# Optimization experiments

Measured on AMD Instinct MI355X. Metric: run time of the kernel, lower is better.

The kernel has to match this reference:

```python
import jax, jax.numpy as jnp
import numpy as np

N_NODES = 100000
N_EDGES = 1600000
IN_F = 64
OUT_F = 32
NEG_SLOPE = 0.2


def setup_inputs() -> dict:
    key = jax.random.key(0)
    k = jax.random.split(key, 6)
    x = jax.random.normal(k[0], (N_NODES, IN_F), dtype=jnp.float32)
    edge_index = jax.random.randint(k[1], (2, N_EDGES), 0, N_NODES, dtype=jnp.int64)
    W = jax.random.normal(k[2], (IN_F, OUT_F), dtype=jnp.float32) * 0.1
    att_src = jax.random.normal(k[3], (OUT_F,), dtype=jnp.float32) * 0.1
    att_dst = jax.random.normal(k[4], (OUT_F,), dtype=jnp.float32) * 0.1
    bias = jax.random.normal(k[5], (OUT_F,), dtype=jnp.float32) * 0.1
    return {"x": x, "edge_index": edge_index, "W": W,
            "att_src": att_src, "att_dst": att_dst, "bias": bias}


def reference(x, edge_index, W, att_src, att_dst, bias):
    N = x.shape[0]
    # Linear projection (single head, concat=True -> [N, OUT_F])
    h = x @ W  # [N, C]
    a_src = h @ att_src  # [N] per-node source attention logit contribution
    a_dst = h @ att_dst  # [N] per-node destination contribution
    # add self loops (PyG GATConv default add_self_loops=True)
    loop = jnp.arange(N, dtype=edge_index.dtype)
    src = jnp.concatenate([edge_index[0], loop])  # [E+N] message senders
    dst = jnp.concatenate([edge_index[1], loop])  # [E+N] message receivers
    # attention logits per edge, LeakyReLU(alpha_src[j] + alpha_dst[i])
    e = jax.nn.leaky_relu(a_src[src] + a_dst[dst], NEG_SLOPE)
    # segment softmax over incoming edges of each destination node
    m = jax.ops.segment_max(e, dst, num_segments=N)  # every node has a self loop
    ex = jnp.exp(e - m[dst])
    denom = jax.ops.segment_sum(ex, dst, num_segments=N)
    alpha = ex / denom[dst]  # [E+N]
    # weighted scatter-add of source features into destinations
    out = jax.ops.segment_sum(h[src] * alpha[:, None], dst, num_segments=N)
    out = out + bias
    # GATLayer activation='relu'
    return jax.nn.relu(out)
```

## Files before the change

kernel.cpp:

```cpp
#include <hip/hip_runtime.h>
#include <hip/hip_fp16.h>
#include <math.h>

#define IN_F 64
#define OUT_F 32
#define NEG_SLOPE 0.2f

#define BK_SHIFT 7
#define BK 128
#define NBMAX 1024
#define NBLKA 256
#define PSTAGE 10

typedef _Float16 half8_t __attribute__((ext_vector_type(8)));
typedef float float4_t __attribute__((ext_vector_type(4)));

__device__ __forceinline__ float leaky(float v) {
    return (v > 0.0f) ? v : NEG_SLOPE * v;
}

__device__ __forceinline__ int incScan256(int v, int tid, int* wsum) {
    const int lane = tid & 63, wid = tid >> 6;
    #pragma unroll
    for (int m = 1; m < 64; m <<= 1) {
        int u = __shfl_up(v, m);
        if (lane >= m) v += u;
    }
    if (lane == 63) wsum[wid] = v;
    __syncthreads();
    int add = 0;
    for (int k = 0; k < wid; ++k) add += wsum[k];
    __syncthreads();
    return v + add;
}

__device__ __forceinline__ int incScan512(int v, int tid, int* wsum) {
    const int lane = tid & 63, wid = tid >> 6;
    #pragma unroll
    for (int m = 1; m < 64; m <<= 1) {
        int u = __shfl_up(v, m);
        if (lane >= m) v += u;
    }
    if (lane == 63) wsum[wid] = v;
    __syncthreads();
    int add = 0;
    for (int k = 0; k < wid; ++k) add += wsum[k];
    __syncthreads();
    return v + add;
}

__global__ __launch_bounds__(256) void k_projhist(
        const float* __restrict__ x, const float* __restrict__ W,
        const float* __restrict__ att_src, const float* __restrict__ att_dst,
        __half2* __restrict__ h2, float* __restrict__ asrc, float* __restrict__ adst,
        const int* __restrict__ dst, int* __restrict__ hist,
        int N, int NB, int E, int epb, int PB) {
    __shared__ int smem[2560];
    const int tid = threadIdx.x;

    if (blockIdx.x >= PB) {
        int* lh = smem;
        const int blk = blockIdx.x - PB;
        for (int i = tid; i < NB; i += 256) lh[i] = 0;
        __syncthreads();
        const int e0 = blk * epb, e1 = min(E, e0 + epb);
        for (int e = e0 + tid; e < e1; e += 256) atomicAdd(&lh[dst[e] >> BK_SHIFT], 1);
        __syncthreads();
        for (int b = tid; b < NB; b += 256) hist[(size_t)b * NBLKA + blk] = lh[b];
        return;
    }

    const int wv   = tid >> 6;
    const int lane = tid & 63;
    const int m    = lane & 15;
    const int quad = lane >> 4;
    const int node0 = (blockIdx.x * 4 + wv) * 16;
    if (node0 >= N) return;

    const int kb = quad * 8;
    half8_t b00, b01, b10, b11;
    #pragma unroll
    for (int j = 0; j < 8; ++j) {
        b00[j] = (_Float16)W[(kb + j) * OUT_F + m];
        b01[j] = (_Float16)W[(32 + kb + j) * OUT_F + m];
        b10[j] = (_Float16)W[(kb + j) * OUT_F + 16 + m];
        b11[j] = (_Float16)W[(32 + kb + j) * OUT_F + 16 + m];
    }
    const int row = min(node0 + m, N - 1);
    const float* xr = x + (size_t)row * IN_F + kb;
    float4_t xa = *(const float4_t*)(xr);
    float4_t xb = *(const float4_t*)(xr + 4);
    float4_t xc = *(const float4_t*)(xr + 32);
    float4_t xd = *(const float4_t*)(xr + 36);
    half8_t a0, a1;
    #pragma unroll
    for (int j = 0; j < 4; ++j) {
        a0[j] = (_Float16)xa[j]; a0[4 + j] = (_Float16)xb[j];
        a1[j] = (_Float16)xc[j]; a1[4 + j] = (_Float16)xd[j];
    }
    float4_t acc0 = {0.f, 0.f, 0.f, 0.f};
    float4_t acc1 = {0.f, 0.f, 0.f, 0.f};
    acc0 = __builtin_amdgcn_mfma_f32_16x16x32_f16(a0, b00, acc0, 0, 0, 0);
    acc0 = __builtin_amdgcn_mfma_f32_16x16x32_f16(a1, b01, acc0, 0, 0, 0);
    acc1 = __builtin_amdgcn_mfma_f32_16x16x32_f16(a0, b10, acc1, 0, 0, 0);
    acc1 = __builtin_amdgcn_mfma_f32_16x16x32_f16(a1, b11, acc1, 0, 0, 0);

    const float aS0 = att_src[m], aS1 = att_src[16 + m];
    const float aD0 = att_dst[m], aD1 = att_dst[16 + m];
    #pragma unroll
    for (int r = 0; r < 4; ++r) {
        const int node = node0 + quad * 4 + r;
        float h0 = acc0[r], h1 = acc1[r];
        float h0p = __shfl_xor(h0, 1);
        float h1p = __shfl_xor(h1, 1);
        if (node < N && (m & 1) == 0) {
            __half2 hv;
            hv.x = __float2half_rn(h0); hv.y = __float2half_rn(h0p);
            h2[(size_t)node * 16 + (m >> 1)] = hv;
            __half2 hw;
            hw.x = __float2half_rn(h1); hw.y = __float2half_rn(h1p);
            h2[(size_t)node * 16 + 8 + (m >> 1)] = hw;
        }
        float vs = h0 * aS0 + h1 * aS1;
        float vd = h0 * aD0 + h1 * aD1;
        #pragma unroll
        for (int mm = 1; mm < 16; mm <<= 1) {
            vs += __shfl_xor(vs, mm);
            vd += __shfl_xor(vd, mm);
        }
        if (node < N && m == 0) {
            asrc[node] = vs;
            adst[node] = vd;
        }
    }
}

__global__ __launch_bounds__(256) void k_scan1(int* __restrict__ hist,
                                               int* __restrict__ bsum, int NB) {
    __shared__ int wsum[4];
    const int b = blockIdx.x, tid = threadIdx.x;
    int v = hist[(size_t)b * NBLKA + tid];
    const int inc = incScan256(v, tid, wsum);
    hist[(size_t)b * NBLKA + tid] = inc - v;
    if (tid == 255) bsum[b] = inc;
}

__global__ __launch_bounds__(512) void k_bpart(const int* __restrict__ src,
                                               const int* __restrict__ dst,
                                               const int* __restrict__ hist,
                                               const int* __restrict__ bsum,
                                               int* __restrict__ recs,
                                               int NB, int E, int epb) {
    __shared__ int tt[NBMAX];
    __shared__ int lcur[NBMAX];
    __shared__ int wsum[8];
    const int tid = threadIdx.x, blk = blockIdx.x;
    for (int i = tid; i < NBMAX; i += 512) tt[i] = (i < NB) ? bsum[i] : 0;
    __syncthreads();
    {
        int a0 = tt[tid * 2], a1 = tt[tid * 2 + 1];
        int s = a0 + a1;
        int inc = incScan512(s, tid, wsum);
        int run = inc - s;
        tt[tid * 2] = run; run += a0;
        tt[tid * 2 + 1] = run;
    }
    __syncthreads();
    for (int b = tid; b < NB; b += 512)
        lcur[b] = hist[(size_t)b * NBLKA + blk] + tt[b];
    __syncthreads();
    const int e0 = blk * epb, e1 = min(E, e0 + epb);
    for (int e = e0 + tid; e < e1; e += 512) {
        int s = src[e];
        int d = dst[e];
        int p = atomicAdd(&lcur[d >> BK_SHIFT], 1);
        recs[p] = ((d & (BK - 1)) << 17) | s;
    }
}

__global__ __launch_bounds__(256) void k_place(const int* __restrict__ recs,
                                               const int* __restrict__ bsum,
                                               int* __restrict__ cnt,
                                               int* __restrict__ offs,
                                               int* __restrict__ col,
                                               int NB, int E, int N) {
    __shared__ int tt[NBMAX];
    __shared__ int fineCnt[BK];
    __shared__ int cur[BK];
    __shared__ int wsum[4];
    const int b = blockIdx.x, tid = threadIdx.x;
    for (int i = tid; i < NBMAX; i += 256) tt[i] = (i < NB) ? bsum[i] : 0;
    __syncthreads();
    {
        int a0 = tt[tid * 4], a1 = tt[tid * 4 + 1], a2 = tt[tid * 4 + 2], a3 = tt[tid * 4 + 3];
        int s = a0 + a1 + a2 + a3;
        int inc = incScan256(s, tid, wsum);
        int run = inc - s;
        tt[tid * 4] = run;     run += a0;
        tt[tid * 4 + 1] = run; run += a1;
        tt[tid * 4 + 2] = run; run += a2;
        tt[tid * 4 + 3] = run;
    }
    __syncthreads();
    const int cb0 = tt[b];
    const int cb1 = (b + 1 < NB) ? tt[b + 1] : E;
    const int count = cb1 - cb0;
    int myrec[PSTAGE];
    if (tid < BK) fineCnt[tid] = 0;
    __syncthreads();
    #pragma unroll
    for (int k = 0; k < PSTAGE; ++k) {
        int i = tid + k * 256;
        if (i < count) {
            int v = recs[cb0 + i];
            myrec[k] = v;
            atomicAdd(&fineCnt[v >> 17], 1);
        }
    }
    for (int i = tid + PSTAGE * 256; i < count; i += 256)
        atomicAdd(&fineCnt[recs[cb0 + i] >> 17], 1);
    __syncthreads();
    const int v0 = (tid < BK) ? fineCnt[tid] : 0;
    const int inc = incScan256(v0, tid, wsum);
    const int excl = inc - v0;
    if (tid < BK) {
        const int node = (b << BK_SHIFT) + tid;
        if (node < N) {
            cnt[node]  = v0;
            offs[node] = cb0 + excl;
        }
        cur[tid] = cb0 + excl;
    }
    __syncthreads();
    #pragma unroll
    for (int k = 0; k < PSTAGE; ++k) {
        int i = tid + k * 256;
        if (i < count) {
            int r = myrec[k];
            int p = atomicAdd(&cur[r >> 17], 1);
            col[p] = r & 0x1FFFF;
        }
    }
    for (int i = tid + PSTAGE * 256; i < count; i += 256) {
        int r = recs[cb0 + i];
        int p = atomicAdd(&cur[r >> 17], 1);
        col[p] = r & 0x1FFFF;
    }
}

__global__ void k_gather(const int* __restrict__ col, const int* __restrict__ offs,
                         const int* __restrict__ cnt, const float* __restrict__ asrc,
                         const float* __restrict__ adst, const __half2* __restrict__ h2,
                         const float* __restrict__ bias, float* __restrict__ out, int N) {
    int t = blockIdx.x * 256 + threadIdx.x;
    int n = t >> 6;
    if (n >= N) return;
    const int lane = t & 63;
    const int g  = lane >> 4;
    const int c2 = lane & 15;
    const float adst_n = adst[n];
    float l = 0.0f, accx = 0.0f, accy = 0.0f;
    if (g == 0) {
        float p = __expf(leaky(asrc[n] + adst_n));
        float2 hv = __half22float2(h2[(size_t)n * 16 + c2]);
        l = p; accx = p * hv.x; accy = p * hv.y;
    }
    const int off = offs[n];
    const int deg = cnt[n];
    const int q = (deg + 3) >> 2;
    int j = off + g * q;
    const int jend = min(j + q, off + deg);
    for (; j < jend; j += 4) {
        const int last = jend - 1;
        int i1 = min(j + 1, last), i2 = min(j + 2, last), i3 = min(j + 3, last);
        int s0 = col[j], s1 = col[i1], s2 = col[i2], s3 = col[i3];
        float a0 = asrc[s0], a1 = asrc[s1], a2 = asrc[s2], a3 = asrc[s3];
        float2 h0 = __half22float2(h2[(size_t)s0 * 16 + c2]);
        float2 h1 = __half22float2(h2[(size_t)s1 * 16 + c2]);
        float2 hv2 = __half22float2(h2[(size_t)s2 * 16 + c2]);
        float2 h3 = __half22float2(h2[(size_t)s3 * 16 + c2]);
        float p0 = __expf(leaky(a0 + adst_n));
        float p1 = (j + 1 < jend) ? __expf(leaky(a1 + adst_n)) : 0.0f;
        float p2 = (j + 2 < jend) ? __expf(leaky(a2 + adst_n)) : 0.0f;
        float p3 = (j + 3 < jend) ? __expf(leaky(a3 + adst_n)) : 0.0f;
        l += (p0 + p1) + (p2 + p3);
        accx += p0 * h0.x + p1 * h1.x + p2 * hv2.x + p3 * h3.x;
        accy += p0 * h0.y + p1 * h1.y + p2 * hv2.y + p3 * h3.y;
    }
    l    += __shfl_xor(l, 16);    l    += __shfl_xor(l, 32);
    accx += __shfl_xor(accx, 16); accx += __shfl_xor(accx, 32);
    accy += __shfl_xor(accy, 16); accy += __shfl_xor(accy, 32);
    if (g == 0) {
        float inv = 1.0f / l;
        float2 bb = ((const float2*)bias)[c2];
        float2 o;
        o.x = fmaxf(accx * inv + bb.x, 0.0f);
        o.y = fmaxf(accy * inv + bb.y, 0.0f);
        ((float2*)out)[(size_t)n * 16 + c2] = o;
    }
}

extern "C" void kernel_launch(void* const* d_in, const int* in_sizes, int n_in,
                              void* d_out, int out_size, void* d_ws, size_t ws_size,
                              hipStream_t stream) {
    const float* x        = (const float*)d_in[0];
    const int*   eidx     = (const int*)d_in[1];
    const float* W        = (const float*)d_in[2];
    const float* att_src  = (const float*)d_in[3];
    const float* att_dst  = (const float*)d_in[4];
    const float* bias     = (const float*)d_in[5];
    float* out = (float*)d_out;

    const int N = in_sizes[0] / IN_F;
    const int E = in_sizes[1] / 2;
    const int* src = eidx;
    const int* dst = eidx + E;

    const int NB  = (N + BK - 1) >> BK_SHIFT;
    const int epb = (E + NBLKA - 1) / NBLKA;

    int* u = (int*)d_ws;
    size_t o = 0;
    __half2* h2   = (__half2*)(u + o); o += (size_t)N * 16;
    float*   asrc = (float*)(u + o);   o += N;
    float*   adst = (float*)(u + o);   o += N;
    int*     cnt  = u + o;             o += N;
    int*     offs = u + o;             o += N;
    int*     hist = u + o;             o += (size_t)NB * NBLKA;
    int*     bsum = u + o;             o += NBMAX;
    int*     col  = u + o;             o += E;
    int*     recs = u + o;             o += E;

    const int PB = (N + 63) / 64;
    const int gatherBlocks = ((size_t)N * 64 + 255) / 256;

    k_projhist<<<PB + NBLKA, 256, 0, stream>>>(x, W, att_src, att_dst, h2, asrc, adst,
                                               dst, hist, N, NB, E, epb, PB);
    k_scan1<<<NB, 256, 0, stream>>>(hist, bsum, NB);
    k_bpart<<<NBLKA, 512, 0, stream>>>(src, dst, hist, bsum, recs, NB, E, epb);
    k_place<<<NB, 256, 0, stream>>>(recs, bsum, cnt, offs, col, NB, E, N);
    k_gather<<<gatherBlocks, 256, 0, stream>>>(col, offs, cnt, asrc, adst, h2, bias, out, N);
}
```

Baseline: 169.0 us.

## Replace fine CSR placement and gather with bucket-level shared-memory atomic aggregation

```diff
diff --git a/kernel.cpp b/kernel.cpp
--- a/kernel.cpp
+++ b/kernel.cpp
@@ -10,13 +10,18 @@
 #define BK 128
 #define NBMAX 1024
 #define NBLKA 256
-#define PSTAGE 10
 
 typedef _Float16 half8_t __attribute__((ext_vector_type(8)));
 typedef float float4_t __attribute__((ext_vector_type(4)));
+typedef int int4_t __attribute__((ext_vector_type(4)));
 
 __device__ __forceinline__ float leaky(float v) {
     return (v > 0.0f) ? v : NEG_SLOPE * v;
+}
+
+__device__ __forceinline__ float2 h2f(int w) {
+    __half2 h = *reinterpret_cast<__half2*>(&w);
+    return __half22float2(h);
 }
 
 __device__ __forceinline__ int incScan256(int v, int tid, int* wsum) {
@@ -150,6 +155,7 @@
                                                const int* __restrict__ hist,
                                                const int* __restrict__ bsum,
                                                int* __restrict__ recs,
+                                               int* __restrict__ boff,
                                                int NB, int E, int epb) {
     __shared__ int tt[NBMAX];
     __shared__ int lcur[NBMAX];
@@ -166,6 +172,10 @@
         tt[tid * 2 + 1] = run;
     }
     __syncthreads();
+    if (blk == 0) {
+        for (int b = tid; b < NB; b += 512) boff[b] = tt[b];
+        if (tid == 0) boff[NB] = E;
+    }
     for (int b = tid; b < NB; b += 512)
         lcur[b] = hist[(size_t)b * NBLKA + blk] + tt[b];
     __syncthreads();
@@ -178,125 +188,75 @@
     }
 }
 
-__global__ __launch_bounds__(256) void k_place(const int* __restrict__ recs,
-                                               const int* __restrict__ bsum,
-                                               int* __restrict__ cnt,
-                                               int* __restrict__ offs,
-                                               int* __restrict__ col,
-                                               int NB, int E, int N) {
-    __shared__ int tt[NBMAX];
-    __shared__ int fineCnt[BK];
-    __shared__ int cur[BK];
-    __shared__ int wsum[4];
+__global__ __launch_bounds__(512) void k_agg(const int* __restrict__ recs,
+                                             const int* __restrict__ boff,
+                                             const float* __restrict__ asrc,
+                                             const float* __restrict__ adst,
+                                             const __half2* __restrict__ h2,
+                                             const float* __restrict__ bias,
+                                             float* __restrict__ out,
+                                             int NB, int E, int N) {
+    __shared__ float acc[BK * 33];
+    __shared__ float adl[BK];
     const int b = blockIdx.x, tid = threadIdx.x;
-    for (int i = tid; i < NBMAX; i += 256) tt[i] = (i < NB) ? bsum[i] : 0;
-    __syncthreads();
-    {
-        int a0 = tt[tid * 4], a1 = tt[tid * 4 + 1], a2 = tt[tid * 4 + 2], a3 = tt[tid * 4 + 3];
-        int s = a0 + a1 + a2 + a3;
-        int inc = incScan256(s, tid, wsum);
-        int run = inc - s;
-        tt[tid * 4] = run;     run += a0;
-        tt[tid * 4 + 1] = run; run += a1;
-        tt[tid * 4 + 2] = run; run += a2;
-        tt[tid * 4 + 3] = run;
-    }
-    __syncthreads();
-    const int cb0 = tt[b];
-    const int cb1 = (b + 1 < NB) ? tt[b + 1] : E;
-    const int count = cb1 - cb0;
-    int myrec[PSTAGE];
-    if (tid < BK) fineCnt[tid] = 0;
-    __syncthreads();
-    #pragma unroll
-    for (int k = 0; k < PSTAGE; ++k) {
-        int i = tid + k * 256;
-        if (i < count) {
-            int v = recs[cb0 + i];
-            myrec[k] = v;
-            atomicAdd(&fineCnt[v >> 17], 1);
-        }
-    }
-    for (int i = tid + PSTAGE * 256; i < count; i += 256)
-        atomicAdd(&fineCnt[recs[cb0 + i] >> 17], 1);
-    __syncthreads();
-    const int v0 = (tid < BK) ? fineCnt[tid] : 0;
-    const int inc = incScan256(v0, tid, wsum);
-    const int excl = inc - v0;
+    const int node0 = b << BK_SHIFT;
+
+    for (int i = tid; i < BK * 33; i += 512) acc[i] = 0.0f;
     if (tid < BK) {
-        const int node = (b << BK_SHIFT) + tid;
-        if (node < N) {
-            cnt[node]  = v0;
-            offs[node] = cb0 + excl;
-        }
-        cur[tid] = cb0 + excl;
-    }
-    __syncthreads();
-    #pragma unroll
-    for (int k = 0; k < PSTAGE; ++k) {
-        int i = tid + k * 256;
-        if (i < count) {
-            int r = myrec[k];
-            int p = atomicAdd(&cur[r >> 17], 1);
-            col[p] = r & 0x1FFFF;
-        }
-    }
-    for (int i = tid + PSTAGE * 256; i < count; i += 256) {
-        int r = recs[cb0 + i];
-        int p = atomicAdd(&cur[r >> 17], 1);
-        col[p] = r & 0x1FFFF;
-    }
-}
-
-__global__ void k_gather(const int* __restrict__ col, const int* __restrict__ offs,
-                         const int* __restrict__ cnt, const float* __restrict__ asrc,
-                         const float* __restrict__ adst, const __half2* __restrict__ h2,
-                         const float* __restrict__ bias, float* __restrict__ out, int N) {
-    int t = blockIdx.x * 256 + threadIdx.x;
-    int n = t >> 6;
-    if (n >= N) return;
-    const int lane = t & 63;
-    const int g  = lane >> 4;
-    const int c2 = lane & 15;
-    const float adst_n = adst[n];
-    float l = 0.0f, accx = 0.0f, accy = 0.0f;
-    if (g == 0) {
-        float p = __expf(leaky(asrc[n] + adst_n));
-        float2 hv = __half22float2(h2[(size_t)n * 16 + c2]);
-        l = p; accx = p * hv.x; accy = p * hv.y;
-    }
-    const int off = offs[n];
-    const int deg = cnt[n];
-    const int q = (deg + 3) >> 2;
-    int j = off + g * q;
-    const int jend = min(j + q, off + deg);
-    for (; j < jend; j += 4) {
-        const int last = jend - 1;
-        int i1 = min(j + 1, last), i2 = min(j + 2, last), i3 = min(j + 3, last);
-        int s0 = col[j], s1 = col[i1], s2 = col[i2], s3 = col[i3];
-        float a0 = asrc[s0], a1 = asrc[s1], a2 = asrc[s2], a3 = asrc[s3];
-        float2 h0 = __half22float2(h2[(size_t)s0 * 16 + c2]);
-        float2 h1 = __half22float2(h2[(size_t)s1 * 16 + c2]);
-        float2 hv2 = __half22float2(h2[(size_t)s2 * 16 + c2]);
-        float2 h3 = __half22float2(h2[(size_t)s3 * 16 + c2]);
-        float p0 = __expf(leaky(a0 + adst_n));
-        float p1 = (j + 1 < jend) ? __expf(leaky(a1 + adst_n)) : 0.0f;
-        float p2 = (j + 2 < jend) ? __expf(leaky(a2 + adst_n)) : 0.0f;
-        float p3 = (j + 3 < jend) ? __expf(leaky(a3 + adst_n)) : 0.0f;
-        l += (p0 + p1) + (p2 + p3);
-        accx += p0 * h0.x + p1 * h1.x + p2 * hv2.x + p3 * h3.x;
-        accy += p0 * h0.y + p1 * h1.y + p2 * hv2.y + p3 * h3.y;
-    }
-    l    += __shfl_xor(l, 16);    l    += __shfl_xor(l, 32);
-    accx += __shfl_xor(accx, 16); accx += __shfl_xor(accx, 32);
-    accy += __shfl_xor(accy, 16); accy += __shfl_xor(accy, 32);
-    if (g == 0) {
-        float inv = 1.0f / l;
-        float2 bb = ((const float2*)bias)[c2];
-        float2 o;
-        o.x = fmaxf(accx * inv + bb.x, 0.0f);
-        o.y = fmaxf(accy * inv + bb.y, 0.0f);
-        ((float2*)out)[(size_t)n * 16 + c2] = o;
+        const int n = node0 + tid;
+        adl[tid] = (n < N) ? adst[n] : 0.0f;
+    }
+    __syncthreads();
+
+    const int cb0 = boff[b];
+    const int cb1 = boff[b + 1];
+
+    int i = cb0 + tid;
+    int r = (i < cb1) ? recs[i] : 0;
+    while (i < cb1) {
+        const int inext = i + 512;
+        const int rn = (inext < cb1) ? recs[inext] : 0;
+        const int s = r & 0x1FFFF;
+        const int d = r >> 17;
+        const int4_t* hp = (const int4_t*)(h2 + (size_t)s * 16);
+        const int4_t q0 = hp[0], q1 = hp[1], q2 = hp[2], q3 = hp[3];
+        const float p = __expf(leaky(asrc[s] + adl[d]));
+        float* accd = acc + d * 33;
+        unsafeAtomicAdd(accd + 32, p);
+        #pragma unroll
+        for (int k = 0; k < 4; ++k) {
+            const int4_t q = (k == 0) ? q0 : (k == 1) ? q1 : (k == 2) ? q2 : q3;
+            #pragma unroll
+            for (int j = 0; j < 4; ++j) {
+                const float2 f = h2f(q[j]);
+                unsafeAtomicAdd(accd + (k * 4 + j) * 2,     p * f.x);
+                unsafeAtomicAdd(accd + (k * 4 + j) * 2 + 1, p * f.y);
+            }
+        }
+        i = inext; r = rn;
+    }
+    __syncthreads();
+
+    const int d  = tid >> 2;
+    const int cb = (tid & 3) * 8;
+    const int n  = node0 + d;
+    if (n < N) {
+        const float ps = __expf(leaky(asrc[n] + adl[d]));
+        const float* accd = acc + d * 33;
+        const float inv = 1.0f / (accd[32] + ps);
+        const int4_t hq = *(const int4_t*)(h2 + (size_t)n * 16 + (cb >> 1));
+        float4_t o0, o1;
+        #pragma unroll
+        for (int k = 0; k < 4; ++k) {
+            const float2 f = h2f(hq[k]);
+            const float v0 = (accd[cb + 2 * k]     + ps * f.x) * inv + bias[cb + 2 * k];
+            const float v1 = (accd[cb + 2 * k + 1] + ps * f.y) * inv + bias[cb + 2 * k + 1];
+            if (k < 2) { o0[2 * k] = fmaxf(v0, 0.0f); o0[2 * k + 1] = fmaxf(v1, 0.0f); }
+            else       { o1[2 * (k - 2)] = fmaxf(v0, 0.0f); o1[2 * (k - 2) + 1] = fmaxf(v1, 0.0f); }
+        }
+        float4_t* op = (float4_t*)(out + (size_t)n * OUT_F + cb);
+        op[0] = o0;
+        op[1] = o1;
     }
 }
 
@@ -324,20 +284,16 @@
     __half2* h2   = (__half2*)(u + o); o += (size_t)N * 16;
     float*   asrc = (float*)(u + o);   o += N;
     float*   adst = (float*)(u + o);   o += N;
-    int*     cnt  = u + o;             o += N;
-    int*     offs = u + o;             o += N;
     int*     hist = u + o;             o += (size_t)NB * NBLKA;
     int*     bsum = u + o;             o += NBMAX;
-    int*     col  = u + o;             o += E;
+    int*     boff = u + o;             o += NBMAX + 1;
     int*     recs = u + o;             o += E;
 
     const int PB = (N + 63) / 64;
-    const int gatherBlocks = ((size_t)N * 64 + 255) / 256;
 
     k_projhist<<<PB + NBLKA, 256, 0, stream>>>(x, W, att_src, att_dst, h2, asrc, adst,
                                                dst, hist, N, NB, E, epb, PB);
     k_scan1<<<NB, 256, 0, stream>>>(hist, bsum, NB);
-    k_bpart<<<NBLKA, 512, 0, stream>>>(src, dst, hist, bsum, recs, NB, E, epb);
-    k_place<<<NB, 256, 0, stream>>>(recs, bsum, cnt, offs, col, NB, E, N);
-    k_gather<<<gatherBlocks, 256, 0, stream>>>(col, offs, cnt, asrc, adst, h2, bias, out, N);
-}
+    k_bpart<<<NBLKA, 512, 0, stream>>>(src, dst, hist, bsum, recs, boff, NB, E, epb);
+    k_agg<<<NB, 512, 0, stream>>>(recs, boff, asrc, adst, h2, bias, out, NB, E, N);
+}
```

New measurement: 465.7 us. 2.76x slower.

## Pad per-node CSR neighbor lists to multiples of 16 with dummy sentinel node

Applied to the files above, without the earlier changes.

```diff
diff --git a/kernel.cpp b/kernel.cpp
--- a/kernel.cpp
+++ b/kernel.cpp
@@ -11,9 +11,12 @@
 #define NBMAX 1024
 #define NBLKA 256
 #define PSTAGE 10
+#define PADSLACK (BK * 15)
 
 typedef _Float16 half8_t __attribute__((ext_vector_type(8)));
 typedef float float4_t __attribute__((ext_vector_type(4)));
+typedef int int4_t __attribute__((ext_vector_type(4)));
+
 
 __device__ __forceinline__ float leaky(float v) {
     return (v > 0.0f) ? v : NEG_SLOPE * v;
@@ -136,9 +139,16 @@
 }
 
 __global__ __launch_bounds__(256) void k_scan1(int* __restrict__ hist,
-                                               int* __restrict__ bsum, int NB) {
+                                               int* __restrict__ bsum,
+                                               __half2* __restrict__ h2,
+                                               float* __restrict__ asrc,
+                                               int N, int NB) {
     __shared__ int wsum[4];
     const int b = blockIdx.x, tid = threadIdx.x;
+    if (b == 0) {
+        if (tid < 16) h2[(size_t)N * 16 + tid] = __floats2half2_rn(0.0f, 0.0f);
+        if (tid == 16) asrc[N] = -1e30f;
+    }
     int v = hist[(size_t)b * NBLKA + tid];
     const int inc = incScan256(v, tid, wsum);
     hist[(size_t)b * NBLKA + tid] = inc - v;
@@ -205,6 +215,8 @@
     const int cb0 = tt[b];
     const int cb1 = (b + 1 < NB) ? tt[b + 1] : E;
     const int count = cb1 - cb0;
+    const int colBase = cb0 + b * PADSLACK;
+    for (int i = tid; i < count + PADSLACK; i += 256) col[colBase + i] = N;
     int myrec[PSTAGE];
     if (tid < BK) fineCnt[tid] = 0;
     __syncthreads();
@@ -221,15 +233,16 @@
         atomicAdd(&fineCnt[recs[cb0 + i] >> 17], 1);
     __syncthreads();
     const int v0 = (tid < BK) ? fineCnt[tid] : 0;
-    const int inc = incScan256(v0, tid, wsum);
-    const int excl = inc - v0;
+    const int pv = (v0 + 15) & ~15;
+    const int pinc = incScan256(pv, tid, wsum);
+    const int pexcl = pinc - pv;
     if (tid < BK) {
         const int node = (b << BK_SHIFT) + tid;
         if (node < N) {
-            cnt[node]  = v0;
-            offs[node] = cb0 + excl;
-        }
-        cur[tid] = cb0 + excl;
+            cnt[node]  = pv;
+            offs[node] = colBase + pexcl;
+        }
+        cur[tid] = colBase + pexcl;
     }
     __syncthreads();
     #pragma unroll
@@ -266,23 +279,20 @@
         l = p; accx = p * hv.x; accy = p * hv.y;
     }
     const int off = offs[n];
-    const int deg = cnt[n];
-    const int q = (deg + 3) >> 2;
-    int j = off + g * q;
-    const int jend = min(j + q, off + deg);
-    for (; j < jend; j += 4) {
-        const int last = jend - 1;
-        int i1 = min(j + 1, last), i2 = min(j + 2, last), i3 = min(j + 3, last);
-        int s0 = col[j], s1 = col[i1], s2 = col[i2], s3 = col[i3];
+    const int q = cnt[n] >> 2;
+    const int j0 = off + g * q;
+    const int jend = j0 + q;
+    for (int j = j0; j < jend; j += 4) {
+        int s0 = col[j], s1 = col[j + 1], s2 = col[j + 2], s3 = col[j + 3];
         float a0 = asrc[s0], a1 = asrc[s1], a2 = asrc[s2], a3 = asrc[s3];
         float2 h0 = __half22float2(h2[(size_t)s0 * 16 + c2]);
         float2 h1 = __half22float2(h2[(size_t)s1 * 16 + c2]);
         float2 hv2 = __half22float2(h2[(size_t)s2 * 16 + c2]);
         float2 h3 = __half22float2(h2[(size_t)s3 * 16 + c2]);
         float p0 = __expf(leaky(a0 + adst_n));
-        float p1 = (j + 1 < jend) ? __expf(leaky(a1 + adst_n)) : 0.0f;
-        float p2 = (j + 2 < jend) ? __expf(leaky(a2 + adst_n)) : 0.0f;
-        float p3 = (j + 3 < jend) ? __expf(leaky(a3 + adst_n)) : 0.0f;
+        float p1 = __expf(leaky(a1 + adst_n));
+        float p2 = __expf(leaky(a2 + adst_n));
+        float p3 = __expf(leaky(a3 + adst_n));
         l += (p0 + p1) + (p2 + p3);
         accx += p0 * h0.x + p1 * h1.x + p2 * hv2.x + p3 * h3.x;
         accy += p0 * h0.y + p1 * h1.y + p2 * hv2.y + p3 * h3.y;
@@ -321,14 +331,14 @@
 
     int* u = (int*)d_ws;
     size_t o = 0;
-    __half2* h2   = (__half2*)(u + o); o += (size_t)N * 16;
-    float*   asrc = (float*)(u + o);   o += N;
+    __half2* h2   = (__half2*)(u + o); o += (size_t)(N + 1) * 16;
+    float*   asrc = (float*)(u + o);   o += N + 1;
     float*   adst = (float*)(u + o);   o += N;
     int*     cnt  = u + o;             o += N;
     int*     offs = u + o;             o += N;
     int*     hist = u + o;             o += (size_t)NB * NBLKA;
     int*     bsum = u + o;             o += NBMAX;
-    int*     col  = u + o;             o += E;
+    int*     col  = u + o;             o += (size_t)E + (size_t)NB * PADSLACK;
     int*     recs = u + o;             o += E;
 
     const int PB = (N + 63) / 64;
@@ -336,7 +346,7 @@
 
     k_projhist<<<PB + NBLKA, 256, 0, stream>>>(x, W, att_src, att_dst, h2, asrc, adst,
                                                dst, hist, N, NB, E, epb, PB);
-    k_scan1<<<NB, 256, 0, stream>>>(hist, bsum, NB);
+    k_scan1<<<NB, 256, 0, stream>>>(hist, bsum, h2, asrc, N, NB);
     k_bpart<<<NBLKA, 512, 0, stream>>>(src, dst, hist, bsum, recs, NB, E, epb);
     k_place<<<NB, 256, 0, stream>>>(recs, bsum, cnt, offs, col, NB, E, N);
     k_gather<<<gatherBlocks, 256, 0, stream>>>(col, offs, cnt, asrc, adst, h2, bias, out, N);
```

Measured after the change: 175.0 us. +3.5%, slower.
